# Kernel tuning notes

Hardware: AMD Instinct MI355X
Metric: run time of the kernel (lower is better)

## Reference

```python
import jax, jax.numpy as jnp
import numpy as np

# Llama-7B FFN up-proj quantized with HQQ 4-bit, group_size=64, axis=0
OUT, IN, GS = 11008, 4096, 64
G = OUT * IN // GS  # 704512 groups


def setup_inputs() -> dict:
    key = jax.random.key(0)
    k1, k2, k3, k4, k5 = jax.random.split(key, 5)
    # packed 4-bit weights: two nibbles per byte, shape [GS//2, G]
    W_q = jax.random.randint(k1, (GS // 2, G), 0, 256, dtype=jnp.int32)
    # per-group scale (meta['scale'] = 1/scale from quantize) and zero
    scale = jax.random.uniform(k2, (1, G), jnp.float32, minval=1e-3, maxval=1e-2)
    zero = jax.random.uniform(k3, (1, G), jnp.float32, minval=0.0, maxval=15.0)
    # decode-style activations: 8 sequences, 1 token each
    x = jax.random.normal(k4, (8, 1, IN), dtype=jnp.float32)
    bias = jax.random.normal(k5, (OUT,), dtype=jnp.float32) * 0.01
    return {"W_q": W_q, "scale": scale, "zero": zero, "x": x, "bias": bias}


def reference(W_q, scale, zero, x, bias):
    # BitPack.unpack_4bit_u8: high nibble rows stacked on low nibble rows
    hi = (W_q >> 4) & 0xF
    lo = W_q & 0xF
    W_q_p = jnp.concatenate([hi, lo], axis=0).astype(x.dtype)  # [GS, G]
    # Quantizer.dequantize: (W_q_p - zero) * scale, reshape to weight shape
    W_r = ((W_q_p - zero) * scale).reshape(OUT, IN)  # [out, in]
    # torch.nn.functional.linear(x, W_r, bias)
    return jnp.einsum('bsi,oi->bso', x, W_r) + bias
```

## Files before the change

### kernel.cpp

```cpp
#include <hip/hip_runtime.h>


#define OUT_ 11008
#define IN_ 4096
#define G_ 704512
#define OC_ 172
#define KS 2
#define KC (IN_ / KS)
#define ITERS (KC / 256)

__global__ __launch_bounds__(256, 2)
void hqq_gemv(const int* __restrict__ Wq, const float* __restrict__ scale,
              const float* __restrict__ zero, const float* __restrict__ x,
              float* __restrict__ ws) {
    __shared__ float s_lds[KC];
    __shared__ float z_lds[KC];
    __shared__ float x_lds[8 * KC];

    const int lane = threadIdx.x;
    const int ty   = threadIdx.y;
    const int tid  = ty * 64 + lane;
    const int oc   = blockIdx.y;
    const int ks   = blockIdx.z;
    const int rq0  = blockIdx.x * 8 + ty * 2;

    const int kbase = ks * KC;
    const long gb = (long)oc * IN_ + kbase;

#pragma unroll
    for (int r = 0; r < KC / 1024; ++r) {
        const int off = r * 1024 + tid * 4;
        *(float4*)(s_lds + off) = *(const float4*)(scale + gb + off);
        *(float4*)(z_lds + off) = *(const float4*)(zero + gb + off);
    }
#pragma unroll
    for (int r = 0; r < 8 * KC / 1024; ++r) {
        const int off = r * 1024 + tid * 4;
        const int b = off >> 11;
        const int k = off & (KC - 1);
        *(float4*)(x_lds + off) = *(const float4*)(x + b * IN_ + kbase + k);
    }

    const int* __restrict__ wqA = Wq + (long)rq0 * G_ + gb;
    const int* __restrict__ wqB = wqA + G_;
    int4 qA[ITERS], qB[ITERS];
#pragma unroll
    for (int it = 0; it < ITERS; ++it) {
        qA[it] = *(const int4*)(wqA + it * 256 + lane * 4);
        qB[it] = *(const int4*)(wqB + it * 256 + lane * 4);
    }

    __syncthreads();

    float acc[4][8];
#pragma unroll
    for (int r = 0; r < 4; ++r)
#pragma unroll
        for (int b = 0; b < 8; ++b) acc[r][b] = 0.f;

#pragma unroll
    for (int it = 0; it < ITERS; ++it) {
        const int i = it * 256 + lane * 4;
        const float4 s4 = *(const float4*)(s_lds + i);
        const float4 z4 = *(const float4*)(z_lds + i);
        const float ss[4] = {s4.x, s4.y, s4.z, s4.w};
        const float zs[4] = {-z4.x * s4.x, -z4.y * s4.y, -z4.z * s4.z, -z4.w * s4.w};
        const int qsA[4] = {qA[it].x, qA[it].y, qA[it].z, qA[it].w};
        const int qsB[4] = {qB[it].x, qB[it].y, qB[it].z, qB[it].w};

        float w[4][4];
#pragma unroll
        for (int j = 0; j < 4; ++j) {
            w[0][j] = fmaf((float)((qsA[j] >> 4) & 0xF), ss[j], zs[j]);
            w[1][j] = fmaf((float)( qsA[j]       & 0xF), ss[j], zs[j]);
            w[2][j] = fmaf((float)((qsB[j] >> 4) & 0xF), ss[j], zs[j]);
            w[3][j] = fmaf((float)( qsB[j]       & 0xF), ss[j], zs[j]);
        }
#pragma unroll
        for (int b = 0; b < 8; ++b) {
            const float4 xb = *(const float4*)(x_lds + b * KC + i);
#pragma unroll
            for (int r = 0; r < 4; ++r) {
                float a = acc[r][b];
                a = fmaf(xb.x, w[r][0], a);
                a = fmaf(xb.y, w[r][1], a);
                a = fmaf(xb.z, w[r][2], a);
                a = fmaf(xb.w, w[r][3], a);
                acc[r][b] = a;
            }
        }
    }

#pragma unroll
    for (int r = 0; r < 4; ++r)
#pragma unroll
        for (int b = 0; b < 8; ++b) {
            float v = acc[r][b];
#pragma unroll
            for (int off = 32; off > 0; off >>= 1)
                v += __shfl_down(v, off, 64);
            acc[r][b] = v;
        }

    if (lane == 0) {
        const int o[4] = {rq0 * OC_ + oc, (rq0 + 32) * OC_ + oc,
                          (rq0 + 1) * OC_ + oc, (rq0 + 33) * OC_ + oc};
        float* __restrict__ wp = ws + (long)ks * 8 * OUT_;
#pragma unroll
        for (int r = 0; r < 4; ++r)
#pragma unroll
            for (int b = 0; b < 8; ++b)
                wp[b * OUT_ + o[r]] = acc[r][b];
    }
}

__global__ void hqq_reduce(const float* __restrict__ ws,
                           const float* __restrict__ bias,
                           float* __restrict__ out) {
    const int t = blockIdx.x * 256 + threadIdx.x;
    if (t >= 8 * OUT_) return;
    const int o = t % OUT_;
    float v = bias[o];
#pragma unroll
    for (int k = 0; k < KS; ++k) v += ws[k * 8 * OUT_ + t];
    out[t] = v;
}

extern "C" void kernel_launch(void* const* d_in, const int* in_sizes, int n_in,
                              void* d_out, int out_size, void* d_ws, size_t ws_size,
                              hipStream_t stream) {
    const int*   Wq    = (const int*)d_in[0];
    const float* scale = (const float*)d_in[1];
    const float* zero  = (const float*)d_in[2];
    const float* x     = (const float*)d_in[3];
    const float* bias  = (const float*)d_in[4];
    float* out = (float*)d_out;
    float* ws  = (float*)d_ws;

    dim3 grid(4, OC_, KS);
    dim3 block(64, 4);
    hqq_gemv<<<grid, block, 0, stream>>>(Wq, scale, zero, x, ws);
    hqq_reduce<<<(8 * OUT_ + 255) / 256, 256, 0, stream>>>(ws, bias, out);
}
```

Measured before the change: 152.2 us.

## Replace LDS staging with per-wave register double-buffered global loads

The kernel no longer stages scale, zero and activations through shared memory behind a block barrier. Each block is now a single wave that reads scale, zero, x and packed weights straight from global memory, prefetching the next iteration's data into registers while computing the current one. The grid grows fourfold to keep the same amount of work. The aim is to remove the LDS fill, the barrier and shared-memory occupancy limits. In exchange, scale, zero and x are now fetched redundantly by every wave and rely on the cache, and register pressure rises from the duplicated prefetch buffers.

```diff
diff --git a/kernel.cpp b/kernel.cpp
--- a/kernel.cpp
+++ b/kernel.cpp
@@ -9,48 +9,22 @@
 #define KC (IN_ / KS)
 #define ITERS (KC / 256)
 
-__global__ __launch_bounds__(256, 2)
+__global__ __launch_bounds__(64, 3)
 void hqq_gemv(const int* __restrict__ Wq, const float* __restrict__ scale,
               const float* __restrict__ zero, const float* __restrict__ x,
               float* __restrict__ ws) {
-    __shared__ float s_lds[KC];
-    __shared__ float z_lds[KC];
-    __shared__ float x_lds[8 * KC];
-
     const int lane = threadIdx.x;
-    const int ty   = threadIdx.y;
-    const int tid  = ty * 64 + lane;
     const int oc   = blockIdx.y;
     const int ks   = blockIdx.z;
-    const int rq0  = blockIdx.x * 8 + ty * 2;
+    const int rq0  = blockIdx.x * 2;
 
     const int kbase = ks * KC;
     const long gb = (long)oc * IN_ + kbase;
-
-#pragma unroll
-    for (int r = 0; r < KC / 1024; ++r) {
-        const int off = r * 1024 + tid * 4;
-        *(float4*)(s_lds + off) = *(const float4*)(scale + gb + off);
-        *(float4*)(z_lds + off) = *(const float4*)(zero + gb + off);
-    }
-#pragma unroll
-    for (int r = 0; r < 8 * KC / 1024; ++r) {
-        const int off = r * 1024 + tid * 4;
-        const int b = off >> 11;
-        const int k = off & (KC - 1);
-        *(float4*)(x_lds + off) = *(const float4*)(x + b * IN_ + kbase + k);
-    }
-
     const int* __restrict__ wqA = Wq + (long)rq0 * G_ + gb;
     const int* __restrict__ wqB = wqA + G_;
-    int4 qA[ITERS], qB[ITERS];
-#pragma unroll
-    for (int it = 0; it < ITERS; ++it) {
-        qA[it] = *(const int4*)(wqA + it * 256 + lane * 4);
-        qB[it] = *(const int4*)(wqB + it * 256 + lane * 4);
-    }
-
-    __syncthreads();
+    const float* __restrict__ sp = scale + gb;
+    const float* __restrict__ zp = zero + gb;
+    const float* __restrict__ xp = x + kbase;
 
     float acc[4][8];
 #pragma unroll
@@ -58,15 +32,36 @@
 #pragma unroll
         for (int b = 0; b < 8; ++b) acc[r][b] = 0.f;
 
+    const int i0 = lane * 4;
+
+    int4  qa = *(const int4*)(wqA + i0);
+    int4  qb = *(const int4*)(wqB + i0);
+    float4 s = *(const float4*)(sp + i0);
+    float4 z = *(const float4*)(zp + i0);
+    float4 xv[8];
+#pragma unroll
+    for (int b = 0; b < 8; ++b)
+        xv[b] = *(const float4*)(xp + b * IN_ + i0);
+
 #pragma unroll
     for (int it = 0; it < ITERS; ++it) {
-        const int i = it * 256 + lane * 4;
-        const float4 s4 = *(const float4*)(s_lds + i);
-        const float4 z4 = *(const float4*)(z_lds + i);
-        const float ss[4] = {s4.x, s4.y, s4.z, s4.w};
-        const float zs[4] = {-z4.x * s4.x, -z4.y * s4.y, -z4.z * s4.z, -z4.w * s4.w};
-        const int qsA[4] = {qA[it].x, qA[it].y, qA[it].z, qA[it].w};
-        const int qsB[4] = {qB[it].x, qB[it].y, qB[it].z, qB[it].w};
+        int4 qa_n, qb_n;
+        float4 s_n, z_n, xv_n[8];
+        if (it + 1 < ITERS) {
+            const int i = i0 + (it + 1) * 256;
+            qa_n = *(const int4*)(wqA + i);
+            qb_n = *(const int4*)(wqB + i);
+            s_n  = *(const float4*)(sp + i);
+            z_n  = *(const float4*)(zp + i);
+#pragma unroll
+            for (int b = 0; b < 8; ++b)
+                xv_n[b] = *(const float4*)(xp + b * IN_ + i);
+        }
+
+        const float ss[4] = {s.x, s.y, s.z, s.w};
+        const float zs[4] = {-z.x * s.x, -z.y * s.y, -z.z * s.z, -z.w * s.w};
+        const int qsA[4] = {qa.x, qa.y, qa.z, qa.w};
+        const int qsB[4] = {qb.x, qb.y, qb.z, qb.w};
 
         float w[4][4];
 #pragma unroll
@@ -78,7 +73,7 @@
         }
 #pragma unroll
         for (int b = 0; b < 8; ++b) {
-            const float4 xb = *(const float4*)(x_lds + b * KC + i);
+            const float4 xb = xv[b];
 #pragma unroll
             for (int r = 0; r < 4; ++r) {
                 float a = acc[r][b];
@@ -88,6 +83,12 @@
                 a = fmaf(xb.w, w[r][3], a);
                 acc[r][b] = a;
             }
+        }
+
+        if (it + 1 < ITERS) {
+            qa = qa_n; qb = qb_n; s = s_n; z = z_n;
+#pragma unroll
+            for (int b = 0; b < 8; ++b) xv[b] = xv_n[b];
         }
     }
 
@@ -137,8 +138,8 @@
     float* out = (float*)d_out;
     float* ws  = (float*)d_ws;
 
-    dim3 grid(4, OC_, KS);
-    dim3 block(64, 4);
+    dim3 grid(16, OC_, KS);
+    dim3 block(64);
     hqq_gemv<<<grid, block, 0, stream>>>(Wq, scale, zero, x, ws);
     hqq_reduce<<<(8 * OUT_ + 255) / 256, 256, 0, stream>>>(ws, bias, out);
 }
```

After: 159.8 us. 1.05x slower.
